# Kernel tuning notes

Hardware: AMD Instinct MI355X
Metric: run time of the kernel (lower is better)

Reference implementation:

```python
import jax, jax.numpy as jnp
import numpy as np

B, S, D, H = 2, 2048, 1024, 16
HSZ = D // H  # 64


def setup_inputs() -> dict:
    key = jax.random.key(0)
    k0, k1, k2, k3, k4 = jax.random.split(key, 5)
    scale = 0.02
    return {
        "x": jax.random.normal(k0, (B, S, D), dtype=jnp.float32),
        "in_proj_w": jax.random.normal(k1, (3 * D, D), dtype=jnp.float32) * scale,
        "in_proj_b": jax.random.normal(k2, (3 * D,), dtype=jnp.float32) * scale,
        "out_proj_w": jax.random.normal(k3, (D, D), dtype=jnp.float32) * scale,
        "out_proj_b": jax.random.normal(k4, (D,), dtype=jnp.float32) * scale,
    }


def reference(x, in_proj_w, in_proj_b, out_proj_w, out_proj_b):
    # Packed QKV projection (self-attention fast path: query is key is value).
    qkv = x @ in_proj_w.T + in_proj_b              # (B, S, 3D)
    q, k, v = jnp.split(qkv, 3, axis=-1)           # each (B, S, D)

    def to_heads(t):
        return t.reshape(B, S, H, HSZ).transpose(0, 2, 1, 3)  # (B, H, S, hsz)

    q, k, v = to_heads(q), to_heads(k), to_heads(v)

    # Causal additive bias: -inf above the diagonal (tril keeps, logical_not masks).
    neg_inf = jnp.float32(-jnp.inf)
    causal = jnp.tril(jnp.ones((S, S), dtype=bool))
    attn_bias = jnp.where(causal, jnp.float32(0.0), neg_inf)  # (S, S)

    inv_sqrt = jnp.float32(1.0 / np.sqrt(HSZ))
    scores = jnp.einsum("bhqd,bhkd->bhqk", q * inv_sqrt, k) + attn_bias
    attn_w = jax.nn.softmax(scores, axis=-1)       # (B, H, S, S)

    out = jnp.einsum("bhqk,bhkd->bhqd", attn_w, v)  # (B, H, S, hsz)
    out = jnp.nan_to_num(out, nan=0.0)              # matches torch.nan_to_num_
    out = out.transpose(0, 2, 1, 3).reshape(B, S, D)  # concat heads
    out = out @ out_proj_w.T + out_proj_b           # (B, S, D)
    return out, attn_w
```

## Files before the change

### kernel.cpp

```cpp
#include <hip/hip_runtime.h>
#include <stdint.h>

typedef __bf16 bf16;
typedef __attribute__((ext_vector_type(8))) __bf16 bf16x8;
typedef __attribute__((ext_vector_type(4))) __bf16 bf16x4;
typedef __attribute__((ext_vector_type(4))) float f32x4;

#define MFMA16(a, b, c) __builtin_amdgcn_mfma_f32_16x16x32_bf16((a), (b), (c), 0, 0, 0)

constexpr int S = 2048, Dm = 1024, HS = 64;
constexpr float SCALE = 0.125f;
constexpr float SHIFT = 8.0f;

__device__ __forceinline__ int ktmax_of(int qt) { return (qt * 64 + 191) >> 7; }

__device__ __forceinline__ void job_decode(int j, int& qt, int& kg) {
  int acc = 0;
  for (int q = 0; q < 32; ++q) {
    const int ng = (ktmax_of(q) + 3) >> 2;
    if (j < acc + ng) { qt = q; kg = j - acc; return; }
    acc += ng;
  }
  qt = 31; kg = 0;
}

__device__ __forceinline__ void gld_lds16(const void* g, void* lds_uniform) {
  __builtin_amdgcn_global_load_lds(
      (const __attribute__((address_space(1))) void*)g,
      (__attribute__((address_space(3))) void*)lds_uniform,
      16, 0, 0);
}

__global__ __launch_bounds__(256) void cvt_kernel(const float* __restrict__ src,
                                                  bf16* __restrict__ dst, int n) {
  int i4 = (blockIdx.x * 256 + threadIdx.x) * 4;
  if (i4 < n) {
    const float4 f = *(const float4*)(src + i4);
    bf16x4 o;
    o[0] = (bf16)f.x; o[1] = (bf16)f.y; o[2] = (bf16)f.z; o[3] = (bf16)f.w;
    *(bf16x4*)(dst + i4) = o;
  }
}

__global__ __launch_bounds__(256) void gemm_bt_kernel(
    const bf16* __restrict__ A, const bf16* __restrict__ Bw,
    const float* __restrict__ bias, void* __restrict__ Cout,
    int N, int K, int out_is_bf16) {
  __shared__ bf16 As[128 * 32];
  __shared__ bf16 Bs[128 * 32];
  const int t = threadIdx.x;
  const int wave = t >> 6, lane = t & 63, quad = lane >> 4, l15 = lane & 15;
  const int wm = wave >> 1, wn = wave & 1;
  const int m0 = blockIdx.y * 128, n0 = blockIdx.x * 128;

  f32x4 acc[4][4];
#pragma unroll
  for (int mt = 0; mt < 4; ++mt)
#pragma unroll
    for (int nt = 0; nt < 4; ++nt) acc[mt][nt] = f32x4{0.f, 0.f, 0.f, 0.f};

  const bf16* Ag = A + (size_t)(m0 + (t >> 2)) * K + (t & 3) * 8;
  const bf16* Bg = Bw + (size_t)(n0 + (t >> 2)) * K + (t & 3) * 8;
  char* AsB = (char*)As;
  char* BsB = (char*)Bs;
  const int woff = wave * 1024;

  for (int k0 = 0; k0 < K; k0 += 32) {
    __syncthreads();
    gld_lds16(Ag + k0, AsB + woff);
    gld_lds16(Ag + (size_t)64 * K + k0, AsB + 4096 + woff);
    gld_lds16(Bg + k0, BsB + woff);
    gld_lds16(Bg + (size_t)64 * K + k0, BsB + 4096 + woff);
    __syncthreads();
    bf16x8 af[4], bfr[4];
#pragma unroll
    for (int mt = 0; mt < 4; ++mt)
      af[mt] = *(const bf16x8*)(As + (wm * 64 + mt * 16 + l15) * 32 + quad * 8);
#pragma unroll
    for (int nt = 0; nt < 4; ++nt)
      bfr[nt] = *(const bf16x8*)(Bs + (wn * 64 + nt * 16 + l15) * 32 + quad * 8);
#pragma unroll
    for (int mt = 0; mt < 4; ++mt)
#pragma unroll
      for (int nt = 0; nt < 4; ++nt)
        acc[mt][nt] = MFMA16(af[mt], bfr[nt], acc[mt][nt]);
  }

#pragma unroll
  for (int mt = 0; mt < 4; ++mt) {
    const int row = m0 + wm * 64 + mt * 16 + quad * 4;
#pragma unroll
    for (int nt = 0; nt < 4; ++nt) {
      const int col = n0 + wn * 64 + nt * 16 + l15;
      const float bcol = bias[col];
#pragma unroll
      for (int r = 0; r < 4; ++r) {
        float v = acc[mt][nt][r] + bcol;
        if (out_is_bf16)
          ((bf16*)Cout)[(size_t)(row + r) * N + col] = (bf16)v;
        else
          ((float*)Cout)[(size_t)(row + r) * N + col] = v;
      }
    }
  }
}

__global__ __launch_bounds__(256) void stats_kernel(const bf16* __restrict__ qkv,
                                                    float* __restrict__ lsum) {
  const int t = threadIdx.x, wave = t >> 6, lane = t & 63, quad = lane >> 4, l15 = lane & 15;
  int qt, kg;
  job_decode(79 - blockIdx.x, qt, kg);
  const int bh = blockIdx.y, b = bh >> 4, h = bh & 15;
  const int q0 = qt * 64;

  const bf16* qbase = qkv + (size_t)b * S * (3 * Dm) + h * HS;
  const bf16* kbase = qbase + Dm;
  const bf16* qrow = qbase + (size_t)(q0 + wave * 16 + l15) * (3 * Dm);
  const bf16x8 qf0 = *(const bf16x8*)(qrow + quad * 8);
  const bf16x8 qf1 = *(const bf16x8*)(qrow + 32 + quad * 8);
  const int rowb = q0 + wave * 16 + quad * 4;

  const int kt0 = kg * 4, kt1 = min(kt0 + 4, ktmax_of(qt));
  float accr[4] = {0.f, 0.f, 0.f, 0.f};

  for (int kt = kt0; kt < kt1; ++kt) {
    const int kc0 = kt * 128;
    f32x4 sacc[8];
#pragma unroll
    for (int nt = 0; nt < 8; ++nt) sacc[nt] = f32x4{0.f, 0.f, 0.f, 0.f};
#pragma unroll
    for (int nt = 0; nt < 8; ++nt) {
      const bf16* krow = kbase + (size_t)(kc0 + nt * 16 + l15) * (3 * Dm);
      const bf16x8 kf0 = *(const bf16x8*)(krow + quad * 8);
      const bf16x8 kf1 = *(const bf16x8*)(krow + 32 + quad * 8);
      sacc[nt] = MFMA16(qf0, kf0, sacc[nt]);
      sacc[nt] = MFMA16(qf1, kf1, sacc[nt]);
    }
#pragma unroll
    for (int nt = 0; nt < 8; ++nt) {
      const int col = kc0 + nt * 16 + l15;
#pragma unroll
      for (int r = 0; r < 4; ++r) {
        if (col <= rowb + r) accr[r] += __expf(sacc[nt][r] * SCALE - SHIFT);
      }
    }
  }
#pragma unroll
  for (int r = 0; r < 4; ++r) {
    float v = accr[r];
#pragma unroll
    for (int off = 1; off < 16; off <<= 1) v += __shfl_xor(v, off, 16);
    if (l15 == 0) atomicAdd(&lsum[bh * S + rowb + r], v);
  }
}

__global__ __launch_bounds__(256) void write_pv_kernel(
    const bf16* __restrict__ qkv, const float* __restrict__ lsum,
    float* __restrict__ attnw, float* __restrict__ Oacc) {
  constexpr int PSF = 132;
  constexpr int VST = 136;
  __shared__ float Ps[64 * PSF];
  __shared__ bf16 Vt[64 * VST];
  const int t = threadIdx.x, wave = t >> 6, lane = t & 63, quad = lane >> 4, l15 = lane & 15;
  int qt, kg;
  job_decode(79 - blockIdx.x, qt, kg);
  const int bh = blockIdx.y, b = bh >> 4, h = bh & 15;
  const int q0 = qt * 64;

  const bf16* qbase = qkv + (size_t)b * S * (3 * Dm) + h * HS;
  const bf16* kbase = qbase + Dm;
  const bf16* vbase = qbase + 2 * Dm;
  const bf16* qrow = qbase + (size_t)(q0 + wave * 16 + l15) * (3 * Dm);
  const bf16x8 qf0 = *(const bf16x8*)(qrow + quad * 8);
  const bf16x8 qf1 = *(const bf16x8*)(qrow + 32 + quad * 8);
  const int rowb = q0 + wave * 16 + quad * 4;

  float rl[4];
#pragma unroll
  for (int r = 0; r < 4; ++r) rl[r] = 1.f / lsum[bh * S + rowb + r];

  f32x4 oacc[4];
#pragma unroll
  for (int nto = 0; nto < 4; ++nto) oacc[nto] = f32x4{0.f, 0.f, 0.f, 0.f};

  float* aw = attnw + ((size_t)bh * S + q0) * S;
  const int kt0 = kg * 4, kt1 = min(kt0 + 4, ktmax_of(qt));

  for (int kt = kt0; kt < kt1; ++kt) {
    const int kc0 = kt * 128;
    __syncthreads();
    {
      ushort* vt = (ushort*)Vt;
#pragma unroll
      for (int it = 0; it < 16; ++it) {
        const int idx = it * 512 + t * 2;
        const int key = idx >> 6, hd = idx & 63;
        const unsigned u =
            *(const unsigned*)(vbase + (size_t)(kc0 + key) * (3 * Dm) + hd);
        vt[hd * VST + key] = (ushort)(u & 0xffffu);
        vt[(hd + 1) * VST + key] = (ushort)(u >> 16);
      }
    }
    f32x4 sacc[8];
#pragma unroll
    for (int nt = 0; nt < 8; ++nt) sacc[nt] = f32x4{0.f, 0.f, 0.f, 0.f};
#pragma unroll
    for (int nt = 0; nt < 8; ++nt) {
      const bf16* krow = kbase + (size_t)(kc0 + nt * 16 + l15) * (3 * Dm);
      const bf16x8 kf0 = *(const bf16x8*)(krow + quad * 8);
      const bf16x8 kf1 = *(const bf16x8*)(krow + 32 + quad * 8);
      sacc[nt] = MFMA16(qf0, kf0, sacc[nt]);
      sacc[nt] = MFMA16(qf1, kf1, sacc[nt]);
    }
#pragma unroll
    for (int nt = 0; nt < 8; ++nt) {
      const int col = kc0 + nt * 16 + l15;
#pragma unroll
      for (int r = 0; r < 4; ++r) {
        const float p = (col <= rowb + r)
                            ? __expf(sacc[nt][r] * SCALE - SHIFT) * rl[r]
                            : 0.f;
        Ps[(wave * 16 + quad * 4 + r) * PSF + nt * 16 + l15] = p;
      }
    }
    __syncthreads();

#pragma unroll
    for (int i = 0; i < 8; ++i) {
      const int idx = i * 256 + lane * 4;
      const int row16 = idx >> 7, col = idx & 127;
      const f32x4 v = *(const f32x4*)(Ps + (wave * 16 + row16) * PSF + col);
      __builtin_nontemporal_store(
          v, (f32x4*)(aw + (size_t)(wave * 16 + row16) * S + kc0 + col));
    }

#pragma unroll
    for (int ks = 0; ks < 4; ++ks) {
      const float* prow = Ps + (wave * 16 + l15) * PSF + ks * 32 + quad * 8;
      const f32x4 p0 = *(const f32x4*)prow;
      const f32x4 p1 = *(const f32x4*)(prow + 4);
      bf16x8 pa;
#pragma unroll
      for (int j = 0; j < 4; ++j) { pa[j] = (bf16)p0[j]; pa[4 + j] = (bf16)p1[j]; }
#pragma unroll
      for (int nto = 0; nto < 4; ++nto) {
        const bf16x8 vb =
            *(const bf16x8*)(Vt + (nto * 16 + l15) * VST + ks * 32 + quad * 8);
        oacc[nto] = MFMA16(pa, vb, oacc[nto]);
      }
    }
  }

#pragma unroll
  for (int nto = 0; nto < 4; ++nto) {
    const int hd = nto * 16 + l15;
#pragma unroll
    for (int r = 0; r < 4; ++r) {
      atomicAdd(&Oacc[((size_t)bh * S + rowb + r) * 64 + hd], oacc[nto][r]);
    }
  }
}

__global__ __launch_bounds__(256) void zf_kernel(float* __restrict__ attnw) {
  const int t = threadIdx.x;
  const int qt = blockIdx.x, bh = blockIdx.y;
  const int c0 = ktmax_of(qt) * 128;
  const int nz = S - c0;
  if (nz <= 0) return;
  const int nv = nz >> 2;
  const int total = 64 * nv;
  float* aw = attnw + ((size_t)bh * S + qt * 64) * S;
  const f32x4 z = {0.f, 0.f, 0.f, 0.f};
  for (int i = t; i < total; i += 256) {
    const int rr = i / nv, cc = i - rr * nv;
    __builtin_nontemporal_store(z, (f32x4*)(aw + (size_t)rr * S + c0 + cc * 4));
  }
}

__global__ __launch_bounds__(256) void ocvt_kernel(const float* __restrict__ Oacc,
                                                   bf16* __restrict__ ho) {
  const int i4 = (blockIdx.x * 256 + threadIdx.x) * 4;
  const int bh = i4 >> 17, rem = i4 & 131071;
  const int row = rem >> 6, hd = rem & 63;
  const int b = bh >> 4, h = bh & 15;
  const float4 f = *(const float4*)(Oacc + i4);
  bf16x4 o;
  o[0] = (bf16)f.x; o[1] = (bf16)f.y; o[2] = (bf16)f.z; o[3] = (bf16)f.w;
  *(bf16x4*)(ho + (size_t)(b * S + row) * Dm + h * HS + hd) = o;
}

extern "C" void kernel_launch(void* const* d_in, const int* in_sizes, int n_in,
                              void* d_out, int out_size, void* d_ws, size_t ws_size,
                              hipStream_t stream) {
  (void)in_sizes; (void)n_in; (void)out_size; (void)ws_size;
  const float* x = (const float*)d_in[0];
  const float* wi = (const float*)d_in[1];
  const float* bi = (const float*)d_in[2];
  const float* wo = (const float*)d_in[3];
  const float* bo = (const float*)d_in[4];

  char* ws = (char*)d_ws;
  bf16* qkv = (bf16*)(ws);
  bf16* ho = (bf16*)(ws + 25165824);
  float* lsum = (float*)(ws + 25165824);
  float* Oacc = (float*)(ws + 33554432);
  bf16* xb = (bf16*)(ws + 33554432);
  bf16* wib = (bf16*)(ws + 41943040);
  bf16* wob = (bf16*)(ws);

  float* out = (float*)d_out;
  float* attnw = out + (size_t)4194304;

  cvt_kernel<<<4096, 256, 0, stream>>>(x, xb, 4194304);
  cvt_kernel<<<3072, 256, 0, stream>>>(wi, wib, 3145728);
  gemm_bt_kernel<<<dim3(24, 32), 256, 0, stream>>>(xb, wib, bi, qkv, 3072, 1024, 1);
  hipMemsetAsync(Oacc, 0, 16777216, stream);
  hipMemsetAsync(lsum, 0, 262144, stream);
  stats_kernel<<<dim3(80, 32), 256, 0, stream>>>(qkv, lsum);
  write_pv_kernel<<<dim3(80, 32), 256, 0, stream>>>(qkv, lsum, attnw, Oacc);
  zf_kernel<<<dim3(32, 32), 256, 0, stream>>>(attnw);
  cvt_kernel<<<1024, 256, 0, stream>>>(wo, wob, 1048576);
  ocvt_kernel<<<4096, 256, 0, stream>>>(Oacc, ho);
  gemm_bt_kernel<<<dim3(8, 32), 256, 0, stream>>>(ho, wob, bo, out, 1024, 1024, 0);
}
```

Before: 858.3 us.

## Pre-transpose V into a global buffer and drop block-wide barriers in PV kernel

Adds a kernel that transposes V per head into a head-dim-major bf16 buffer placed in the output region (later overwritten by the final GEMM). The PV kernel then reads V^T fragments straight from global memory instead of rebuilding a transposed V tile in shared memory for every key tile. Each wave now uses only its own slice of the P scratch, so the two __syncthreads are replaced by per-wave LDS waitcnts. This removes repeated strided transposes and block barriers, at the cost of an extra kernel launch, extra global traffic, and reliance on the out buffer staying free until the final GEMM.

```diff
diff --git a/kernel.cpp b/kernel.cpp
--- a/kernel.cpp
+++ b/kernel.cpp
@@ -105,6 +105,31 @@
   }
 }
 
+__global__ __launch_bounds__(256) void vt_kernel(const bf16* __restrict__ qkv,
+                                                 bf16* __restrict__ VT) {
+  constexpr int VST = 136;
+  __shared__ ushort Vt[64 * VST];
+  const int t = threadIdx.x;
+  const int kc0 = blockIdx.x * 128, bh = blockIdx.y, b = bh >> 4, h = bh & 15;
+  const bf16* vbase = qkv + (size_t)b * S * (3 * Dm) + 2 * Dm + h * HS;
+#pragma unroll
+  for (int it = 0; it < 16; ++it) {
+    const int idx = it * 512 + t * 2;
+    const int key = idx >> 6, hd = idx & 63;
+    const unsigned u = *(const unsigned*)(vbase + (size_t)(kc0 + key) * (3 * Dm) + hd);
+    Vt[hd * VST + key] = (ushort)(u & 0xffffu);
+    Vt[(hd + 1) * VST + key] = (ushort)(u >> 16);
+  }
+  __syncthreads();
+  ushort* o = (ushort*)(VT + (size_t)bh * HS * S + kc0);
+#pragma unroll
+  for (int it = 0; it < 4; ++it) {
+    const int slot = it * 256 + t;
+    const int hd = slot >> 4, kg = slot & 15;
+    *(uint4*)(o + (size_t)hd * S + kg * 8) = *(const uint4*)&Vt[hd * VST + kg * 8];
+  }
+}
+
 __global__ __launch_bounds__(256) void stats_kernel(const bf16* __restrict__ qkv,
                                                     float* __restrict__ lsum) {
   const int t = threadIdx.x, wave = t >> 6, lane = t & 63, quad = lane >> 4, l15 = lane & 15;
@@ -156,11 +181,10 @@
 
 __global__ __launch_bounds__(256) void write_pv_kernel(
     const bf16* __restrict__ qkv, const float* __restrict__ lsum,
-    float* __restrict__ attnw, float* __restrict__ Oacc) {
+    const bf16* __restrict__ VTg, float* __restrict__ attnw,
+    float* __restrict__ Oacc) {
   constexpr int PSF = 132;
-  constexpr int VST = 136;
   __shared__ float Ps[64 * PSF];
-  __shared__ bf16 Vt[64 * VST];
   const int t = threadIdx.x, wave = t >> 6, lane = t & 63, quad = lane >> 4, l15 = lane & 15;
   int qt, kg;
   job_decode(79 - blockIdx.x, qt, kg);
@@ -169,7 +193,7 @@
 
   const bf16* qbase = qkv + (size_t)b * S * (3 * Dm) + h * HS;
   const bf16* kbase = qbase + Dm;
-  const bf16* vbase = qbase + 2 * Dm;
+  const bf16* vt = VTg + (size_t)bh * HS * S;
   const bf16* qrow = qbase + (size_t)(q0 + wave * 16 + l15) * (3 * Dm);
   const bf16x8 qf0 = *(const bf16x8*)(qrow + quad * 8);
   const bf16x8 qf1 = *(const bf16x8*)(qrow + 32 + quad * 8);
@@ -184,23 +208,11 @@
   for (int nto = 0; nto < 4; ++nto) oacc[nto] = f32x4{0.f, 0.f, 0.f, 0.f};
 
   float* aw = attnw + ((size_t)bh * S + q0) * S;
+  float* Pw = Ps + wave * 16 * PSF;
   const int kt0 = kg * 4, kt1 = min(kt0 + 4, ktmax_of(qt));
 
   for (int kt = kt0; kt < kt1; ++kt) {
     const int kc0 = kt * 128;
-    __syncthreads();
-    {
-      ushort* vt = (ushort*)Vt;
-#pragma unroll
-      for (int it = 0; it < 16; ++it) {
-        const int idx = it * 512 + t * 2;
-        const int key = idx >> 6, hd = idx & 63;
-        const unsigned u =
-            *(const unsigned*)(vbase + (size_t)(kc0 + key) * (3 * Dm) + hd);
-        vt[hd * VST + key] = (ushort)(u & 0xffffu);
-        vt[(hd + 1) * VST + key] = (ushort)(u >> 16);
-      }
-    }
     f32x4 sacc[8];
 #pragma unroll
     for (int nt = 0; nt < 8; ++nt) sacc[nt] = f32x4{0.f, 0.f, 0.f, 0.f};
@@ -220,23 +232,23 @@
         const float p = (col <= rowb + r)
                             ? __expf(sacc[nt][r] * SCALE - SHIFT) * rl[r]
                             : 0.f;
-        Ps[(wave * 16 + quad * 4 + r) * PSF + nt * 16 + l15] = p;
+        Pw[(quad * 4 + r) * PSF + nt * 16 + l15] = p;
       }
     }
-    __syncthreads();
+    asm volatile("s_waitcnt lgkmcnt(0)" ::: "memory");
 
 #pragma unroll
     for (int i = 0; i < 8; ++i) {
       const int idx = i * 256 + lane * 4;
       const int row16 = idx >> 7, col = idx & 127;
-      const f32x4 v = *(const f32x4*)(Ps + (wave * 16 + row16) * PSF + col);
+      const f32x4 v = *(const f32x4*)(Pw + row16 * PSF + col);
       __builtin_nontemporal_store(
           v, (f32x4*)(aw + (size_t)(wave * 16 + row16) * S + kc0 + col));
     }
 
 #pragma unroll
     for (int ks = 0; ks < 4; ++ks) {
-      const float* prow = Ps + (wave * 16 + l15) * PSF + ks * 32 + quad * 8;
+      const float* prow = Pw + l15 * PSF + ks * 32 + quad * 8;
       const f32x4 p0 = *(const f32x4*)prow;
       const f32x4 p1 = *(const f32x4*)(prow + 4);
       bf16x8 pa;
@@ -244,11 +256,12 @@
       for (int j = 0; j < 4; ++j) { pa[j] = (bf16)p0[j]; pa[4 + j] = (bf16)p1[j]; }
 #pragma unroll
       for (int nto = 0; nto < 4; ++nto) {
-        const bf16x8 vb =
-            *(const bf16x8*)(Vt + (nto * 16 + l15) * VST + ks * 32 + quad * 8);
+        const bf16x8 vb = *(const bf16x8*)(vt + (size_t)(nto * 16 + l15) * S +
+                                           kc0 + ks * 32 + quad * 8);
         oacc[nto] = MFMA16(pa, vb, oacc[nto]);
       }
     }
+    asm volatile("s_waitcnt lgkmcnt(0)" ::: "memory");
   }
 
 #pragma unroll
@@ -310,14 +323,16 @@
 
   float* out = (float*)d_out;
   float* attnw = out + (size_t)4194304;
+  bf16* VT = (bf16*)d_out;
 
   cvt_kernel<<<4096, 256, 0, stream>>>(x, xb, 4194304);
   cvt_kernel<<<3072, 256, 0, stream>>>(wi, wib, 3145728);
   gemm_bt_kernel<<<dim3(24, 32), 256, 0, stream>>>(xb, wib, bi, qkv, 3072, 1024, 1);
   hipMemsetAsync(Oacc, 0, 16777216, stream);
   hipMemsetAsync(lsum, 0, 262144, stream);
+  vt_kernel<<<dim3(16, 32), 256, 0, stream>>>(qkv, VT);
   stats_kernel<<<dim3(80, 32), 256, 0, stream>>>(qkv, lsum);
-  write_pv_kernel<<<dim3(80, 32), 256, 0, stream>>>(qkv, lsum, attnw, Oacc);
+  write_pv_kernel<<<dim3(80, 32), 256, 0, stream>>>(qkv, lsum, VT, attnw, Oacc);
   zf_kernel<<<dim3(32, 32), 256, 0, stream>>>(attnw);
   cvt_kernel<<<1024, 256, 0, stream>>>(wo, wob, 1048576);
   ocvt_kernel<<<4096, 256, 0, stream>>>(Oacc, ho);
```

Result: no change. 870.5 us (+1.4%).
